# Optimization experiments

Hardware: AMD Instinct MI355X
Metric: run time of the kernel (lower is better)

Reference implementation:

```python
import jax, jax.numpy as jnp
import numpy as np

B, N, T, F_IN = 32, 64, 11, 4
K, H, O, NH = 2, 256, 256, 256  # edge_types, msg_hid, msg_out, n_hid
E = N * (N - 1)


def setup_inputs() -> dict:
    key = jax.random.key(0)
    ks = jax.random.split(key, 16)
    # fully-connected graph without self loops: edge e = (recv i, send j)
    recv = np.array([i for i in range(N) for j in range(N) if i != j])
    send = np.array([j for i in range(N) for j in range(N) if i != j])
    rel_rec = np.zeros((E, N), dtype=np.float32)
    rel_rec[np.arange(E), recv] = 1.0
    rel_send = np.zeros((E, N), dtype=np.float32)
    rel_send[np.arange(E), send] = 1.0

    def lin(k, fan_in, shape):
        return jax.random.normal(k, shape, dtype=jnp.float32) / np.sqrt(fan_in)

    return {
        "inputs": jax.random.normal(ks[0], (B, N, T, F_IN), dtype=jnp.float32),
        "edges": jax.random.uniform(ks[1], (B, E, K), dtype=jnp.float32),
        "rel_rec": jnp.asarray(rel_rec),
        "rel_send": jnp.asarray(rel_send),
        "W1": lin(ks[2], 2 * F_IN, (K, 2 * F_IN, H)),
        "b1": jnp.zeros((K, H), dtype=jnp.float32),
        "W2": lin(ks[3], H, (K, H, O)),
        "b2": jnp.zeros((K, O), dtype=jnp.float32),
        "Wo1": lin(ks[4], F_IN + O, (F_IN + O, NH)),
        "bo1": jnp.zeros((NH,), dtype=jnp.float32),
        "Wo2": lin(ks[5], NH, (NH, NH)),
        "bo2": jnp.zeros((NH,), dtype=jnp.float32),
        "Wo3": lin(ks[6], NH, (NH, F_IN)),
        "bo3": jnp.zeros((F_IN,), dtype=jnp.float32),
        "sample_timesteps": jnp.arange(T, dtype=jnp.float32),
        "pred_steps": 10,
        "scale": 10,
    }


def reference(inputs, edges, rel_rec, rel_send, W1, b1, W2, b2,
              Wo1, bo1, Wo2, bo2, Wo3, bo3, sample_timesteps, pred_steps, scale):
    t = sample_timesteps / scale
    x_all = jnp.transpose(inputs, (0, 2, 1, 3))  # [B, T, N, F]

    def f(x):  # ODE dynamics = single_step_forward (returns x + pred)
        recv = jnp.einsum('en,bnf->bef', rel_rec, x)   # gather receivers
        send = jnp.einsum('en,bnf->bef', rel_send, x)  # gather senders
        pre = jnp.concatenate([send, recv], axis=-1)   # [B, E, 2F]
        m = jax.nn.relu(jnp.einsum('bef,kfh->bkeh', pre, W1) + b1[None, :, None, :])
        m = jax.nn.relu(jnp.einsum('bkeh,kho->bkeo', m, W2) + b2[None, :, None, :])
        all_msgs = jnp.einsum('bkeo,bek->beo', m, edges)  # weighted sum over edge types
        agg = jnp.einsum('beo,en->bno', all_msgs, rel_rec)  # scatter to receivers
        aug = jnp.concatenate([x, agg], axis=-1)
        p = jax.nn.relu(aug @ Wo1 + bo1)
        p = jax.nn.relu(p @ Wo2 + bo2)
        p = p @ Wo3 + bo3
        return x + p

    preds = []
    for idx in range(0, T, pred_steps):
        vt = t[idx:idx + pred_steps + 1]
        if vt.shape[0] == 1:
            continue
        x0 = x_all[:, idx]          # [B, N, F]
        dts = vt[1:] - vt[:-1]      # [steps]

        def rk4(x, dt):
            k1 = f(x)
            k2 = f(x + 0.5 * dt * k1)
            k3 = f(x + 0.5 * dt * k2)
            k4 = f(x + dt * k3)
            xn = x + (dt / 6.0) * (k1 + 2.0 * k2 + 2.0 * k3 + k4)
            return xn, xn

        _, xs = jax.lax.scan(rk4, x0, dts)           # [steps, B, N, F]
        preds.append(jnp.transpose(xs, (1, 0, 2, 3)))  # [B, steps, N, F]

    out = jnp.concatenate(preds, axis=1)
    return jnp.transpose(out, (0, 2, 1, 3))  # [B, N, steps, F]
```

## Files before the change

### kernel.cpp

```cpp
#include <hip/hip_runtime.h>

#define BB 32
#define NN 64
#define TT 11
#define FF 4
#define KK 2
#define EE 4032
#define NSTEP 10

typedef _Float16 f16x8 __attribute__((ext_vector_type(8)));
typedef float    f32x4v __attribute__((ext_vector_type(4)));

#define OFF_U0   0
#define OFF_VB   65536
#define OFF_Y    73728
#define OFF_WGT  74752
#define SMEM2    78848
#define OFF_AUGH 0
#define OFF_P1H  9472
#define OFF_P2   17920

__device__ __forceinline__ float scrub(float v) {
    return fminf(fmaxf(v, -3.0e4f), 3.0e4f);
}

__device__ __forceinline__ float load_dt(const float* ts, const void* scp, int step) {
    float t0 = ts[step], t1 = ts[step + 1];
    int w = ((const int*)scp)[0];
    float scl;
    if (w > 0 && w < 1000000) scl = (float)w;
    else {
        float f = __int_as_float(w);
        scl = (f > 0.5f && f < 1.0e6f) ? f : 10.0f;
    }
    return (t1 - t0) / scl;
}

__device__ __forceinline__ void build_uk(char* smem, int buf, int k, int tid,
    const float* __restrict__ W1g, const float* smY)
{
    int hg = tid & 31, sb = tid >> 5;
    const float* w1p = W1g + k * 2048 + hg * 8;
    f32x4v wA[4], wB[4];
    #pragma unroll
    for (int f = 0; f < 4; ++f) {
        wA[f] = *(const f32x4v*)(w1p + f * 256);
        wB[f] = *(const f32x4v*)(w1p + f * 256 + 4);
    }
    const int swz = (hg * 16) ^ ((sb & 7) << 4);
    char* ub = smem + OFF_U0 + buf * 32768;
    #pragma unroll
    for (int it = 0; it < 4; ++it) {
        int s = sb + it * 16;
        f32x4v yv = *(const f32x4v*)(smY + s * 4);
        f16x8 uv;
        #pragma unroll
        for (int e = 0; e < 4; ++e) {
            float vA = yv[0]*wA[0][e] + yv[1]*wA[1][e] + yv[2]*wA[2][e] + yv[3]*wA[3][e];
            float vB = yv[0]*wB[0][e] + yv[1]*wB[1][e] + yv[2]*wB[2][e] + yv[3]*wB[3][e];
            uv[e]     = (_Float16)vA;
            uv[e + 4] = (_Float16)vB;
        }
        *(f16x8*)(ub + s * 512 + swz) = uv;
    }
}

__device__ __forceinline__ void build_vbh(_Float16* smVBH, int buf, int k, int tid, int r0,
    const float* __restrict__ W1g, const float* __restrict__ b1g, const float* smY)
{
    #pragma unroll
    for (int it = 0; it < 4; ++it) {
        int i = tid + it * 512;
        int rv = i >> 8, h = i & 255;
        float acch = b1g[k * 256 + h];
        #pragma unroll
        for (int f = 0; f < 4; ++f)
            acch += smY[(r0 + rv) * 4 + f] * W1g[k * 2048 + (4 + f) * 256 + h];
        smVBH[buf * 2048 + i] = (_Float16)acch;
    }
}

__device__ __forceinline__ void gemm_half(char* smem, int buf, int k, int rv, int ch2,
    const _Float16* __restrict__ W2F, const float* __restrict__ b2g,
    const float* smWgt,
    int lane, int ln15, int lg, const int* uoff, int xm6,
    float rsum[8])
{
    const _Float16* smVBH = (const _Float16*)(smem + OFF_VB);

    float bv[8];
    #pragma unroll
    for (int ni = 0; ni < 8; ++ni)
        bv[ni] = b2g[k * 256 + ch2 * 128 + ni * 16 + ln15];

    f32x4v acc[4][8];
    #pragma unroll
    for (int mi = 0; mi < 4; ++mi)
        #pragma unroll
        for (int ni = 0; ni < 8; ++ni)
            acc[mi][ni] = (f32x4v){bv[ni], bv[ni], bv[ni], bv[ni]};

    const _Float16* bbase = W2F + ((size_t)((k * 16 + ch2 * 8) * 8)) * 512 + lane * 8;
    const char* ubase = smem + OFF_U0 + buf * 32768;
    const _Float16* vbase = smVBH + buf * 2048 + rv * 256;

    #pragma unroll
    for (int kc = 0; kc < 8; ++kc) {
        f16x8 bfr[8];
        #pragma unroll
        for (int ni = 0; ni < 8; ++ni)
            bfr[ni] = *(const f16x8*)(bbase + (size_t)(ni * 8 + kc) * 512);
        f16x8 vbv = *(const f16x8*)(vbase + kc * 32 + lg * 8);
        const int kco = (kc * 64) ^ xm6;
        f16x8 af[4];
        f16x8 z = {};
        #pragma unroll
        for (int mi = 0; mi < 4; ++mi) {
            f16x8 uv = *(const f16x8*)(ubase + uoff[mi] + kco);
            af[mi] = __builtin_elementwise_max(uv + vbv, z);
        }
        __builtin_amdgcn_s_setprio(1);
        #pragma unroll
        for (int mi = 0; mi < 4; ++mi)
            #pragma unroll
            for (int ni = 0; ni < 8; ++ni)
                acc[mi][ni] = __builtin_amdgcn_mfma_f32_16x16x32_f16(
                    af[mi], bfr[ni], acc[mi][ni], 0, 0, 0);
        __builtin_amdgcn_s_setprio(0);
    }

    #pragma unroll
    for (int mi = 0; mi < 4; ++mi) {
        #pragma unroll
        for (int rr = 0; rr < 4; ++rr) {
            float w = smWgt[k * 512 + rv * 64 + mi * 16 + lg * 4 + rr];
            #pragma unroll
            for (int ni = 0; ni < 8; ++ni)
                rsum[ni] += fmaxf(acc[mi][ni][rr], 0.0f) * w;
        }
    }
}

__global__ __launch_bounds__(512, 2)
void stage_kernel(int stage, int step,
    const float* __restrict__ edges, const float* __restrict__ W1g,
    const float* __restrict__ b1g,   const _Float16* __restrict__ W2F,
    const float* __restrict__ b2g,
    const _Float16* __restrict__ Wo1F, const float* __restrict__ bo1,
    const _Float16* __restrict__ Wo2F, const float* __restrict__ bo2,
    const float* __restrict__ Wo3, const float* __restrict__ bo3,
    const float* __restrict__ ts,  const void* __restrict__ scp,
    const float* __restrict__ xcur, const float* __restrict__ kprev,
    float* __restrict__ kout,
    const float* __restrict__ k1b, const float* __restrict__ k2b,
    const float* __restrict__ k3b,
    float* __restrict__ xnext, float* __restrict__ outp)
{
    extern __shared__ char smem[];
    _Float16* smVBH = (_Float16*)(smem + OFF_VB);
    float*  smY   = (float*)(smem + OFF_Y);
    float*  smWgt = (float*)(smem + OFF_WGT);

    const int tid = threadIdx.x;
    const int b   = blockIdx.x >> 3;
    const int rg  = blockIdx.x & 7;
    const int r0  = rg * 8;

    const float dt = load_dt(ts, scp, step);
    const float cc = (stage == 0) ? 0.0f : ((stage == 3) ? 1.0f : 0.5f);

    if (tid < 256) {
        int gi = (b * NN) * FF + tid;
        float y = xcur[gi];
        if (stage != 0) y += cc * dt * kprev[gi];
        smY[tid] = scrub(y);
    }
    #pragma unroll
    for (int it = 0; it < 2; ++it) {
        int i = tid + it * 512;
        int k = i >> 9, m = i & 511;
        int rv = m >> 6, s = m & 63;
        int r = r0 + rv;
        float w = 0.0f;
        if (s != r) {
            int j = s - (s > r ? 1 : 0);
            w = edges[((size_t)b * EE + r * 63 + j) * KK + k];
        }
        smWgt[i] = w;
    }

    const int lane = tid & 63;
    const int wn   = tid >> 6;
    const int rv   = wn;
    const int ln15 = lane & 15;
    const int lg   = lane >> 4;

    const int xm45 = (ln15 & 3) << 4;
    const int xm6  = (ln15 & 4) << 4;
    int uoff[4];
    #pragma unroll
    for (int mi = 0; mi < 4; ++mi) {
        int s = mi * 16 + ln15;
        uoff[mi] = s * 512 + ((lg * 16) ^ xm45);
    }

    float rsA[8], rsB[8];
    #pragma unroll
    for (int ni = 0; ni < 8; ++ni) { rsA[ni] = 0.0f; rsB[ni] = 0.0f; }

    __syncthreads();

    build_uk(smem, 0, 0, tid, W1g, smY);
    build_vbh(smVBH, 0, 0, tid, r0, W1g, b1g, smY);
    __syncthreads();

    build_uk(smem, 1, 1, tid, W1g, smY);
    build_vbh(smVBH, 1, 1, tid, r0, W1g, b1g, smY);
    gemm_half(smem, 0, 0, rv, 0, W2F, b2g, smWgt, lane, ln15, lg, uoff, xm6, rsA);
    gemm_half(smem, 0, 0, rv, 1, W2F, b2g, smWgt, lane, ln15, lg, uoff, xm6, rsB);
    __syncthreads();
    gemm_half(smem, 1, 1, rv, 0, W2F, b2g, smWgt, lane, ln15, lg, uoff, xm6, rsA);
    gemm_half(smem, 1, 1, rv, 1, W2F, b2g, smWgt, lane, ln15, lg, uoff, xm6, rsB);

    #pragma unroll
    for (int ni = 0; ni < 8; ++ni) {
        rsA[ni] += __shfl_xor(rsA[ni], 16, 64);
        rsA[ni] += __shfl_xor(rsA[ni], 32, 64);
        rsB[ni] += __shfl_xor(rsB[ni], 16, 64);
        rsB[ni] += __shfl_xor(rsB[ni], 32, 64);
    }
    _Float16* smAugH = (_Float16*)(smem + OFF_AUGH);
    if (lane < 16) {
        #pragma unroll
        for (int ni = 0; ni < 8; ++ni) {
            smAugH[rv * 296 + 4   + ni * 16 + ln15] = (_Float16)rsA[ni];
            smAugH[rv * 296 + 132 + ni * 16 + ln15] = (_Float16)rsB[ni];
        }
    } else if (lg == 1 && ln15 < 4) {
        smAugH[rv * 296 + ln15] = (_Float16)smY[(r0 + rv) * 4 + ln15];
    }
    __syncthreads();

    _Float16* smP1H = (_Float16*)(smem + OFF_P1H);
    float*    smP2  = (float*)(smem + OFF_P2);

    const int ot0 = wn * 2, ot1 = ot0 + 1;

    {
        float b0 = bo1[ot0 * 16 + ln15], b1v = bo1[ot1 * 16 + ln15];
        f32x4v a0 = {b0, b0, b0, b0}, a1 = {b1v, b1v, b1v, b1v};
        const _Float16* bb0 = Wo1F + (size_t)(ot0 * 9) * 512 + lane * 8;
        const _Float16* bb1 = Wo1F + (size_t)(ot1 * 9) * 512 + lane * 8;
        #pragma unroll
        for (int kc = 0; kc < 9; ++kc) {
            f16x8 av  = *(const f16x8*)(smAugH + ln15 * 296 + kc * 32 + lg * 8);
            f16x8 bf0 = *(const f16x8*)(bb0 + kc * 512);
            f16x8 bf1 = *(const f16x8*)(bb1 + kc * 512);
            a0 = __builtin_amdgcn_mfma_f32_16x16x32_f16(av, bf0, a0, 0, 0, 0);
            a1 = __builtin_amdgcn_mfma_f32_16x16x32_f16(av, bf1, a1, 0, 0, 0);
        }
        __syncthreads();
        #pragma unroll
        for (int rr = 0; rr < 4; ++rr) {
            int row = lg * 4 + rr;
            smP1H[row * 264 + ot0 * 16 + ln15] = (_Float16)fmaxf(a0[rr], 0.0f);
            smP1H[row * 264 + ot1 * 16 + ln15] = (_Float16)fmaxf(a1[rr], 0.0f);
        }
    }
    __syncthreads();
    {
        float b0 = bo2[ot0 * 16 + ln15], b1v = bo2[ot1 * 16 + ln15];
        f32x4v a0 = {b0, b0, b0, b0}, a1 = {b1v, b1v, b1v, b1v};
        const _Float16* bb0 = Wo2F + (size_t)(ot0 * 8) * 512 + lane * 8;
        const _Float16* bb1 = Wo2F + (size_t)(ot1 * 8) * 512 + lane * 8;
        #pragma unroll
        for (int kc = 0; kc < 8; ++kc) {
            f16x8 av  = *(const f16x8*)(smP1H + ln15 * 264 + kc * 32 + lg * 8);
            f16x8 bf0 = *(const f16x8*)(bb0 + kc * 512);
            f16x8 bf1 = *(const f16x8*)(bb1 + kc * 512);
            a0 = __builtin_amdgcn_mfma_f32_16x16x32_f16(av, bf0, a0, 0, 0, 0);
            a1 = __builtin_amdgcn_mfma_f32_16x16x32_f16(av, bf1, a1, 0, 0, 0);
        }
        #pragma unroll
        for (int rr = 0; rr < 4; ++rr) {
            int row = lg * 4 + rr;
            smP2[row * 256 + ot0 * 16 + ln15] = fmaxf(a0[rr], 0.0f);
            smP2[row * 256 + ot1 * 16 + ln15] = fmaxf(a1[rr], 0.0f);
        }
    }
    __syncthreads();
    {
        int rr = tid >> 6, f = (tid >> 4) & 3, hs = tid & 15;
        float part = 0.0f;
        #pragma unroll
        for (int j = 0; j < 16; ++j) {
            int h = hs + j * 16;
            part += smP2[rr * 256 + h] * Wo3[h * 4 + f];
        }
        part += __shfl_xor(part, 8, 64);
        part += __shfl_xor(part, 4, 64);
        part += __shfl_xor(part, 2, 64);
        part += __shfl_xor(part, 1, 64);
        if (hs == 0) {
            int grow = b * NN + r0 + rr;
            int gi   = grow * 4 + f;
            float y = smY[(r0 + rr) * 4 + f];
            float knew = scrub(y + bo3[f] + part);
            if (stage < 3) {
                kout[gi] = knew;
            } else {
                float xn = scrub(xcur[gi] + (dt * (1.0f / 6.0f)) *
                           (k1b[gi] + 2.0f * k2b[gi] + 2.0f * k3b[gi] + knew));
                xnext[gi] = xn;
                outp[(size_t)grow * NSTEP * FF + step * FF + f] = xn;
            }
        }
    }
}

__global__ void swizzle_w2(const float* __restrict__ W2, _Float16* __restrict__ W2F)
{
    int idx = blockIdx.x * 256 + threadIdx.x;
    int k   = idx >> 16;
    int rem = idx & 65535;
    int ch  = rem >> 9;
    int pos = rem & 511;
    int ot  = ch >> 3, kc = ch & 7;
    int l   = pos >> 3, e = pos & 7;
    int o   = ot * 16 + (l & 15);
    int h   = kc * 32 + (l >> 4) * 8 + e;
    W2F[idx] = (_Float16)W2[(size_t)(k * 256 + h) * 256 + o];
}

__global__ void swizzle_wo1(const float* __restrict__ Wo1, _Float16* __restrict__ Wo1F)
{
    int idx = blockIdx.x * 256 + threadIdx.x;
    int ch = idx >> 9, pos = idx & 511;
    int ot = ch / 9, kc = ch - ot * 9;
    int l = pos >> 3, e = pos & 7;
    int k = kc * 32 + (l >> 4) * 8 + e;
    int o = ot * 16 + (l & 15);
    Wo1F[idx] = (k < 260) ? (_Float16)Wo1[(size_t)k * 256 + o] : (_Float16)0.0f;
}

__global__ void swizzle_wo2(const float* __restrict__ Wo2, _Float16* __restrict__ Wo2F)
{
    int idx = blockIdx.x * 256 + threadIdx.x;
    int ch = idx >> 9, pos = idx & 511;
    int ot = ch >> 3, kc = ch & 7;
    int l = pos >> 3, e = pos & 7;
    int k = kc * 32 + (l >> 4) * 8 + e;
    int o = ot * 16 + (l & 15);
    Wo2F[idx] = (_Float16)Wo2[(size_t)k * 256 + o];
}

__global__ void init_x(const float* __restrict__ inp, float* __restrict__ x0)
{
    int i = blockIdx.x * 256 + threadIdx.x;
    if (i < BB * NN * FF) {
        int f = i & 3, bn = i >> 2;
        x0[i] = scrub(inp[(size_t)(bn * TT) * FF + f]);
    }
}

static int find_input(const int* in_sizes, int n_in, int want, unsigned char* used, int dflt) {
    if (dflt >= 0 && dflt < n_in && in_sizes[dflt] == want && !used[dflt]) { used[dflt] = 1; return dflt; }
    for (int i = 0; i < n_in; ++i)
        if (!used[i] && in_sizes[i] == want) { used[i] = 1; return i; }
    return dflt;
}

extern "C" void kernel_launch(void* const* d_in, const int* in_sizes, int n_in,
                              void* d_out, int out_size, void* d_ws, size_t ws_size,
                              hipStream_t stream)
{
    unsigned char used[64] = {0};
    int iInp = find_input(in_sizes, n_in, BB*NN*TT*FF, used, 0);
    int iEdg = find_input(in_sizes, n_in, BB*EE*KK,    used, 1);
    (void)find_input(in_sizes, n_in, EE*NN, used, 2);
    (void)find_input(in_sizes, n_in, EE*NN, used, 3);
    int iW1  = find_input(in_sizes, n_in, KK*8*256,  used, 4);
    int ib1  = find_input(in_sizes, n_in, KK*256,    used, 5);
    int iW2  = find_input(in_sizes, n_in, KK*256*256,used, 6);
    int ib2  = find_input(in_sizes, n_in, KK*256,    used, 7);
    int iWo1 = find_input(in_sizes, n_in, 260*256,   used, 8);
    int ibo1 = find_input(in_sizes, n_in, 256,       used, 9);
    int iWo2 = find_input(in_sizes, n_in, 256*256,   used, 10);
    int ibo2 = find_input(in_sizes, n_in, 256,       used, 11);
    int iWo3 = find_input(in_sizes, n_in, 256*4,     used, 12);
    int ibo3 = find_input(in_sizes, n_in, 4,         used, 13);
    int iTs  = find_input(in_sizes, n_in, TT,        used, 14);
    (void)find_input(in_sizes, n_in, 1, used, 15);
    int iSc  = find_input(in_sizes, n_in, 1,         used, 16);

    const float* inputs = (const float*)d_in[iInp];
    const float* edges  = (const float*)d_in[iEdg];
    const float* W1  = (const float*)d_in[iW1];
    const float* b1  = (const float*)d_in[ib1];
    const float* W2  = (const float*)d_in[iW2];
    const float* b2  = (const float*)d_in[ib2];
    const float* Wo1 = (const float*)d_in[iWo1];
    const float* bo1 = (const float*)d_in[ibo1];
    const float* Wo2 = (const float*)d_in[iWo2];
    const float* bo2 = (const float*)d_in[ibo2];
    const float* Wo3 = (const float*)d_in[iWo3];
    const float* bo3 = (const float*)d_in[ibo3];
    const float* ts  = (const float*)d_in[iTs];
    const void*  scp = d_in[iSc];

    char* ws = (char*)d_ws;
    _Float16* W2F  = (_Float16*)ws;
    _Float16* Wo1F = (_Float16*)(ws + 262144);
    _Float16* Wo2F = (_Float16*)(ws + 409600);
    float* xA  = (float*)(ws + 540672);
    float* xB  = (float*)(ws + 540672 + 1 * 32768);
    float* k1  = (float*)(ws + 540672 + 2 * 32768);
    float* k2  = (float*)(ws + 540672 + 3 * 32768);
    float* k3  = (float*)(ws + 540672 + 4 * 32768);

    float* outp = (float*)d_out;

    (void)hipFuncSetAttribute((const void*)stage_kernel,
        hipFuncAttributeMaxDynamicSharedMemorySize, SMEM2);

    swizzle_w2<<<dim3(512), dim3(256), 0, stream>>>(W2, W2F);
    swizzle_wo1<<<dim3(288), dim3(256), 0, stream>>>(Wo1, Wo1F);
    swizzle_wo2<<<dim3(256), dim3(256), 0, stream>>>(Wo2, Wo2F);
    init_x<<<dim3(32), dim3(256), 0, stream>>>(inputs, xA);

    float* xc = xA;
    float* xn = xB;
    for (int step = 0; step < NSTEP; ++step) {
        float* kprevs[4] = { xc, k1, k2, k3 };
        float* kouts[4]  = { k1, k2, k3, k3 };
        for (int s = 0; s < 4; ++s) {
            stage_kernel<<<dim3(256), dim3(512), SMEM2, stream>>>(s, step,
                edges, W1, b1, W2F, b2,
                Wo1F, bo1, Wo2F, bo2, Wo3, bo3, ts, scp, xc, kprevs[s],
                kouts[s], k1, k2, k3, xn, outp);
        }
        float* t = xc; xc = xn; xn = t;
    }
}
```

Before: 1.535 ms.

## Stage W2 tiles into LDS with double-buffered async global_load_lds

The W2 weight fragments are no longer read from global memory straight into registers inside the MFMA loop. Each k/half GEMM is split into two 4-chunk phases, and the next B tile is prefetched into a double-buffered LDS region with global_load_lds, so the load overlaps the current phase's compute. The B tile is shared across the 8 waves, where before each wave loaded it separately. The cost is LDS growing from about 79KB to 144KB, which likely drops occupancy from 2 blocks/CU to 1, plus more barriers. A barrier before the P1H writes was also removed.

```diff
diff --git a/kernel.cpp b/kernel.cpp
--- a/kernel.cpp
+++ b/kernel.cpp
@@ -12,10 +12,11 @@
 typedef float    f32x4v __attribute__((ext_vector_type(4)));
 
 #define OFF_U0   0
-#define OFF_VB   65536
-#define OFF_Y    73728
-#define OFF_WGT  74752
-#define SMEM2    78848
+#define OFF_B    65536
+#define OFF_VB   131072
+#define OFF_Y    139264
+#define OFF_WGT  140288
+#define SMEM2    144384
 #define OFF_AUGH 0
 #define OFF_P1H  9472
 #define OFF_P2   17920
@@ -36,6 +37,23 @@
     return (t1 - t0) / scl;
 }
 
+typedef __attribute__((address_space(1))) const unsigned int glb_u32;
+typedef __attribute__((address_space(3))) unsigned int lds_u32;
+__device__ __forceinline__ void gload_lds16(const void* g, void* l) {
+    __builtin_amdgcn_global_load_lds((glb_u32*)g, (lds_u32*)l, 16, 0, 0);
+}
+
+__device__ __forceinline__ void stage_B(char* smem, int bufsel, int k, int ch2, int h,
+    const _Float16* __restrict__ W2F, int wn, const int* srcOff)
+{
+    const char* base = (const char*)W2F
+        + ((size_t)((k * 16 + ch2 * 8) * 8 + h * 4)) * 1024;
+    char* dst = smem + OFF_B + bufsel * 32768 + wn * 1024;
+    #pragma unroll
+    for (int r = 0; r < 4; ++r)
+        gload_lds16(base + srcOff[r], dst + r * 8192);
+}
+
 __device__ __forceinline__ void build_uk(char* smem, int buf, int k, int tid,
     const float* __restrict__ W1g, const float* smY)
 {
@@ -80,36 +98,32 @@
     }
 }
 
-__device__ __forceinline__ void gemm_half(char* smem, int buf, int k, int rv, int ch2,
-    const _Float16* __restrict__ W2F, const float* __restrict__ b2g,
-    const float* smWgt,
-    int lane, int ln15, int lg, const int* uoff, int xm6,
-    float rsum[8])
-{
-    const _Float16* smVBH = (const _Float16*)(smem + OFF_VB);
-
-    float bv[8];
-    #pragma unroll
-    for (int ni = 0; ni < 8; ++ni)
-        bv[ni] = b2g[k * 256 + ch2 * 128 + ni * 16 + ln15];
-
-    f32x4v acc[4][8];
-    #pragma unroll
-    for (int mi = 0; mi < 4; ++mi)
+__device__ __forceinline__ void acc_init(const float* __restrict__ b2g, int k, int ch2,
+                                         int ln15, f32x4v acc[4][8])
+{
+    #pragma unroll
+    for (int ni = 0; ni < 8; ++ni) {
+        float bv = b2g[k * 256 + ch2 * 128 + ni * 16 + ln15];
+        #pragma unroll
+        for (int mi = 0; mi < 4; ++mi)
+            acc[mi][ni] = (f32x4v){bv, bv, bv, bv};
+    }
+}
+
+__device__ __forceinline__ void gemm4(char* smem, int ubuf, int vbuf, int Bbuf, int rv,
+    int kcBase, int lane, int ln15, int lg, const int* uoff, int xm6,
+    f32x4v acc[4][8])
+{
+    const char* ubase = smem + OFF_U0 + ubuf * 32768;
+    const _Float16* vbase = (const _Float16*)(smem + OFF_VB) + vbuf * 2048 + rv * 256;
+    const char* Bbase = smem + OFF_B + Bbuf * 32768;
+    #pragma unroll
+    for (int kc2 = 0; kc2 < 4; ++kc2) {
+        const int kc = kcBase + kc2;
+        f16x8 bfr[8];
         #pragma unroll
         for (int ni = 0; ni < 8; ++ni)
-            acc[mi][ni] = (f32x4v){bv[ni], bv[ni], bv[ni], bv[ni]};
-
-    const _Float16* bbase = W2F + ((size_t)((k * 16 + ch2 * 8) * 8)) * 512 + lane * 8;
-    const char* ubase = smem + OFF_U0 + buf * 32768;
-    const _Float16* vbase = smVBH + buf * 2048 + rv * 256;
-
-    #pragma unroll
-    for (int kc = 0; kc < 8; ++kc) {
-        f16x8 bfr[8];
-        #pragma unroll
-        for (int ni = 0; ni < 8; ++ni)
-            bfr[ni] = *(const f16x8*)(bbase + (size_t)(ni * 8 + kc) * 512);
+            bfr[ni] = *(const f16x8*)(Bbase + (ni * 4 + kc2) * 1024 + lane * 16);
         f16x8 vbv = *(const f16x8*)(vbase + kc * 32 + lg * 8);
         const int kco = (kc * 64) ^ xm6;
         f16x8 af[4];
@@ -128,9 +142,13 @@
                     af[mi], bfr[ni], acc[mi][ni], 0, 0, 0);
         __builtin_amdgcn_s_setprio(0);
     }
-
-    #pragma unroll
-    for (int mi = 0; mi < 4; ++mi) {
+}
+
+__device__ __forceinline__ void epi(const float* smWgt, int k, int rv, int lg,
+    const f32x4v acc[4][8], float rsum[8])
+{
+    #pragma unroll
+    for (int mi = 0; mi < 4; ++mi)
         #pragma unroll
         for (int rr = 0; rr < 4; ++rr) {
             float w = smWgt[k * 512 + rv * 64 + mi * 16 + lg * 4 + rr];
@@ -138,7 +156,6 @@
             for (int ni = 0; ni < 8; ++ni)
                 rsum[ni] += fmaxf(acc[mi][ni][rr], 0.0f) * w;
         }
-    }
 }
 
 __global__ __launch_bounds__(512, 2)
@@ -179,8 +196,8 @@
     for (int it = 0; it < 2; ++it) {
         int i = tid + it * 512;
         int k = i >> 9, m = i & 511;
-        int rv = m >> 6, s = m & 63;
-        int r = r0 + rv;
+        int rv2 = m >> 6, s = m & 63;
+        int r = r0 + rv2;
         float w = 0.0f;
         if (s != r) {
             int j = s - (s > r ? 1 : 0);
@@ -203,24 +220,65 @@
         int s = mi * 16 + ln15;
         uoff[mi] = s * 512 + ((lg * 16) ^ xm45);
     }
+    int srcOff[4];
+    #pragma unroll
+    for (int r = 0; r < 4; ++r) {
+        int u = r * 512 + tid;
+        int c = u >> 6, w = u & 63;
+        srcOff[r] = ((c >> 2) * 8 + (c & 3)) * 1024 + w * 16;
+    }
 
     float rsA[8], rsB[8];
     #pragma unroll
     for (int ni = 0; ni < 8; ++ni) { rsA[ni] = 0.0f; rsB[ni] = 0.0f; }
+    f32x4v acc[4][8];
 
     __syncthreads();
 
     build_uk(smem, 0, 0, tid, W1g, smY);
     build_vbh(smVBH, 0, 0, tid, r0, W1g, b1g, smY);
-    __syncthreads();
-
+    stage_B(smem, 0, 0, 0, 0, W2F, wn, srcOff);
+    __syncthreads();
+
+    stage_B(smem, 1, 0, 0, 1, W2F, wn, srcOff);
     build_uk(smem, 1, 1, tid, W1g, smY);
     build_vbh(smVBH, 1, 1, tid, r0, W1g, b1g, smY);
-    gemm_half(smem, 0, 0, rv, 0, W2F, b2g, smWgt, lane, ln15, lg, uoff, xm6, rsA);
-    gemm_half(smem, 0, 0, rv, 1, W2F, b2g, smWgt, lane, ln15, lg, uoff, xm6, rsB);
-    __syncthreads();
-    gemm_half(smem, 1, 1, rv, 0, W2F, b2g, smWgt, lane, ln15, lg, uoff, xm6, rsA);
-    gemm_half(smem, 1, 1, rv, 1, W2F, b2g, smWgt, lane, ln15, lg, uoff, xm6, rsB);
+    acc_init(b2g, 0, 0, ln15, acc);
+    gemm4(smem, 0, 0, 0, rv, 0, lane, ln15, lg, uoff, xm6, acc);
+    __syncthreads();
+
+    stage_B(smem, 0, 0, 1, 0, W2F, wn, srcOff);
+    gemm4(smem, 0, 0, 1, rv, 4, lane, ln15, lg, uoff, xm6, acc);
+    epi(smWgt, 0, rv, lg, acc, rsA);
+    __syncthreads();
+
+    stage_B(smem, 1, 0, 1, 1, W2F, wn, srcOff);
+    acc_init(b2g, 0, 1, ln15, acc);
+    gemm4(smem, 0, 0, 0, rv, 0, lane, ln15, lg, uoff, xm6, acc);
+    __syncthreads();
+
+    stage_B(smem, 0, 1, 0, 0, W2F, wn, srcOff);
+    gemm4(smem, 0, 0, 1, rv, 4, lane, ln15, lg, uoff, xm6, acc);
+    epi(smWgt, 0, rv, lg, acc, rsB);
+    __syncthreads();
+
+    stage_B(smem, 1, 1, 0, 1, W2F, wn, srcOff);
+    acc_init(b2g, 1, 0, ln15, acc);
+    gemm4(smem, 1, 1, 0, rv, 0, lane, ln15, lg, uoff, xm6, acc);
+    __syncthreads();
+
+    stage_B(smem, 0, 1, 1, 0, W2F, wn, srcOff);
+    gemm4(smem, 1, 1, 1, rv, 4, lane, ln15, lg, uoff, xm6, acc);
+    epi(smWgt, 1, rv, lg, acc, rsA);
+    __syncthreads();
+
+    stage_B(smem, 1, 1, 1, 1, W2F, wn, srcOff);
+    acc_init(b2g, 1, 1, ln15, acc);
+    gemm4(smem, 1, 1, 0, rv, 0, lane, ln15, lg, uoff, xm6, acc);
+    __syncthreads();
+
+    gemm4(smem, 1, 1, 1, rv, 4, lane, ln15, lg, uoff, xm6, acc);
+    epi(smWgt, 1, rv, lg, acc, rsB);
 
     #pragma unroll
     for (int ni = 0; ni < 8; ++ni) {
@@ -259,7 +317,6 @@
             a0 = __builtin_amdgcn_mfma_f32_16x16x32_f16(av, bf0, a0, 0, 0, 0);
             a1 = __builtin_amdgcn_mfma_f32_16x16x32_f16(av, bf1, a1, 0, 0, 0);
         }
-        __syncthreads();
         #pragma unroll
         for (int rr = 0; rr < 4; ++rr) {
             int row = lg * 4 + rr;
```

New measurement: 1.509 ms. About the same (-1.7%).
